# Performance work log

Hardware: AMD Instinct MI355X
Metric: run time of the kernel (lower is better)

The kernel has to match this reference:

```python
import jax, jax.numpy as jnp
import numpy as np

STEP = 5
ALPHA = 0.01
D = 1024
BN_EPS = 1e-5
L2_EPS = 1e-12


def setup_inputs() -> dict:
    key = jax.random.key(0)
    k1, k2 = jax.random.split(key, 2)
    B = 16
    x = jax.random.normal(k1, (B * STEP, D), dtype=jnp.float32)
    W = jax.random.normal(k2, (D, D), dtype=jnp.float32) * 0.02
    b = jnp.zeros((D,), jnp.float32)
    gamma = jnp.ones((D,), jnp.float32)
    beta = jnp.zeros((D,), jnp.float32)
    return {"x": x, "W": W, "b": b, "gamma": gamma, "beta": beta}


def reference(x, W, b, gamma, beta):
    BS = x.shape[0]          # B * STEP
    B = BS // STEP
    x_seq = x.reshape(B, STEP, D)

    def step_fn(h, xt):
        # xt: [B, D]; Hebbian fast-weight update
        # hebb = alpha * (k v^T - k^2 * h)
        hebb = ALPHA * (xt[:, :, None] * xt[:, None, :] - (xt ** 2)[:, :, None] * h)
        h = h + hebb
        return h, h

    h0 = jnp.zeros((B, D, D), x.dtype)
    _, mems = jax.lax.scan(step_fn, h0, jnp.swapaxes(x_seq, 0, 1))  # [STEP, B, D, D]
    # torch.cat(memory_total, dim=0) -> step-major stacking
    mem = mems.reshape(BS, D, D)

    # batched mat-vec readout; x here is batch-major (faithful to original mismatch)
    q = jnp.einsum('nij,nj->ni', mem, x)  # [BS, D]

    y = q @ W.T + b
    # BatchNorm1d in training mode: batch statistics, biased variance
    mu = y.mean(axis=0)
    var = y.var(axis=0)
    yhat = (y - mu) / jnp.sqrt(var + BN_EPS)
    out = jax.nn.relu(yhat * gamma + beta)
    # F.normalize: L2 over dim=1 with eps clamp
    norm = jnp.linalg.norm(out, axis=1, keepdims=True)
    return out / jnp.maximum(norm, L2_EPS)
```

## Files before the change

### kernel.cpp

```cpp
#include <hip/hip_runtime.h>
#include <hip/hip_bf16.h>
#include <math.h>

#define D_DIM   1024
#define BS      80
#define BATCH   16
#define STEPS   5
#define ALPHA   0.01f
#define BN_EPS  1e-5f
#define L2_EPS  1e-12f

#define K2_NN   8
#define K2_NG   (BS / K2_NN)

__global__ __launch_bounds__(256) void k1_q(const float* __restrict__ x,
                                            float* __restrict__ q,
                                            float* __restrict__ colsum,
                                            float* __restrict__ colsumsq) {
    const int n    = blockIdx.x;
    const int tid  = threadIdx.x;
    const int lane = tid & 63;
    const int wid  = tid >> 6;
    const int t    = n >> 4;
    const int bb   = n & 15;

    if (n < 8) {
        colsum  [n * 256 + tid] = 0.f;
    } else if (n < 16) {
        colsumsq[(n - 8) * 256 + tid] = 0.f;
    }

    const float4* __restrict__ xv = (const float4*)(x + (size_t)n * D_DIM);
    const float4 v = xv[tid];

    float4 k[STEPS];
#pragma unroll
    for (int s = 0; s < STEPS; ++s)
        k[s] = ((const float4*)(x + (size_t)(bb * STEPS + s) * D_DIM))[tid];

    float p[STEPS];
#pragma unroll
    for (int s = 0; s < STEPS; ++s)
        p[s] = k[s].x * v.x + k[s].y * v.y + k[s].z * v.z + k[s].w * v.w;

#pragma unroll
    for (int off = 32; off; off >>= 1) {
#pragma unroll
        for (int s = 0; s < STEPS; ++s) p[s] += __shfl_xor(p[s], off, 64);
    }

    __shared__ float sh[4][STEPS];
    if (lane == 0) {
#pragma unroll
        for (int s = 0; s < STEPS; ++s) sh[wid][s] = p[s];
    }
    __syncthreads();
    float c[STEPS];
#pragma unroll
    for (int s = 0; s < STEPS; ++s)
        c[s] = sh[0][s] + sh[1][s] + sh[2][s] + sh[3][s];

    float4 acc = make_float4(0.f, 0.f, 0.f, 0.f);
    for (int s = 0; s <= t; ++s) {
        const float4 xs = k[s];
        acc.x = acc.x * (1.f - ALPHA * xs.x * xs.x) + c[s] * xs.x;
        acc.y = acc.y * (1.f - ALPHA * xs.y * xs.y) + c[s] * xs.y;
        acc.z = acc.z * (1.f - ALPHA * xs.z * xs.z) + c[s] * xs.z;
        acc.w = acc.w * (1.f - ALPHA * xs.w * xs.w) + c[s] * xs.w;
    }
    acc.x *= ALPHA; acc.y *= ALPHA; acc.z *= ALPHA; acc.w *= ALPHA;
    ((float4*)(q + (size_t)n * D_DIM))[tid] = acc;
}

__global__ __launch_bounds__(256) void k2_gemm(const float* __restrict__ q,
                                               const float* __restrict__ W,
                                               const float* __restrict__ bvec,
                                               float* __restrict__ y,
                                               float* __restrict__ colsum,
                                               float* __restrict__ colsumsq) {
    const int tid  = threadIdx.x;
    const int lane = tid & 63;
    const int wid  = tid >> 6;
    const int wave = blockIdx.x * 4 + wid;
    const int jg   = wave & 255;
    const int ng   = wave >> 8;
    const int j0   = jg * 4;
    const int n0   = ng * K2_NN;

    const float4* __restrict__ W4 = (const float4*)W;
    const float4* __restrict__ q4 = (const float4*)q;

    float4 w[4][4];
#pragma unroll
    for (int jj = 0; jj < 4; ++jj)
#pragma unroll
        for (int m = 0; m < 4; ++m)
            w[jj][m] = W4[(size_t)(j0 + jj) * 256 + lane + 64 * m];

    const float4 b4 = ((const float4*)bvec)[jg];

    float csum[4] = {0.f, 0.f, 0.f, 0.f};
    float csq [4] = {0.f, 0.f, 0.f, 0.f};

#pragma unroll 2
    for (int nn = 0; nn < K2_NN; ++nn) {
        const int n = n0 + nn;
        float4 qv[4];
#pragma unroll
        for (int m = 0; m < 4; ++m)
            qv[m] = q4[(size_t)n * 256 + lane + 64 * m];

        float s[4] = {0.f, 0.f, 0.f, 0.f};
#pragma unroll
        for (int jj = 0; jj < 4; ++jj) {
#pragma unroll
            for (int m = 0; m < 4; ++m) {
                s[jj] += w[jj][m].x * qv[m].x + w[jj][m].y * qv[m].y
                       + w[jj][m].z * qv[m].z + w[jj][m].w * qv[m].w;
            }
        }
#pragma unroll
        for (int off = 32; off; off >>= 1) {
#pragma unroll
            for (int jj = 0; jj < 4; ++jj) s[jj] += __shfl_xor(s[jj], off, 64);
        }
        if (lane == 0) {
            float4 yv = make_float4(s[0] + b4.x, s[1] + b4.y,
                                    s[2] + b4.z, s[3] + b4.w);
            ((float4*)y)[(size_t)n * 256 + jg] = yv;
            csum[0] += yv.x; csum[1] += yv.y; csum[2] += yv.z; csum[3] += yv.w;
            csq[0] += yv.x * yv.x; csq[1] += yv.y * yv.y;
            csq[2] += yv.z * yv.z; csq[3] += yv.w * yv.w;
        }
    }
    if (lane == 0) {
#pragma unroll
        for (int jj = 0; jj < 4; ++jj) {
            atomicAdd(&colsum [j0 + jj], csum[jj]);
            atomicAdd(&colsumsq[j0 + jj], csq[jj]);
        }
    }
}

__global__ __launch_bounds__(256) void k4_norm(const float* __restrict__ y,
                                               const float* __restrict__ colsum,
                                               const float* __restrict__ colsumsq,
                                               const float* __restrict__ gamma,
                                               const float* __restrict__ beta,
                                               float* __restrict__ out) {
    const int n   = blockIdx.x;
    const int tid = threadIdx.x;

    const float inv_bs = 1.f / (float)BS;

    float o[4];
    float ss = 0.f;
#pragma unroll
    for (int m = 0; m < 4; ++m) {
        const int j = tid + 256 * m;
        const float mu   = colsum[j] * inv_bs;
        const float var  = colsumsq[j] * inv_bs - mu * mu;
        const float istd = rsqrtf(var + BN_EPS);
        float v = (y[(size_t)n * D_DIM + j] - mu) * istd * gamma[j] + beta[j];
        v = fmaxf(v, 0.f);
        o[m] = v;
        ss += v * v;
    }

#pragma unroll
    for (int off = 32; off; off >>= 1) ss += __shfl_xor(ss, off, 64);
    __shared__ float sred[4];
    if ((tid & 63) == 0) sred[tid >> 6] = ss;
    __syncthreads();
    const float stot = sred[0] + sred[1] + sred[2] + sred[3];

    const float scale = 1.f / fmaxf(sqrtf(stot), L2_EPS);
#pragma unroll
    for (int m = 0; m < 4; ++m)
        out[(size_t)n * D_DIM + tid + 256 * m] = o[m] * scale;
}

extern "C" void kernel_launch(void* const* d_in, const int* in_sizes, int n_in,
                              void* d_out, int out_size, void* d_ws, size_t ws_size,
                              hipStream_t stream) {
    const float* x     = (const float*)d_in[0];
    const float* W     = (const float*)d_in[1];
    const float* bvec  = (const float*)d_in[2];
    const float* gamma = (const float*)d_in[3];
    const float* beta  = (const float*)d_in[4];

    float* q        = (float*)d_ws;
    float* y        = q + BS * D_DIM;
    float* colsum   = y + BS * D_DIM;
    float* colsumsq = colsum + D_DIM;

    float* out = (float*)d_out;

    k1_q   <<<BS,                    256, 0, stream>>>(x, q, colsum, colsumsq);
    k2_gemm<<<(256 * K2_NG) / 4,     256, 0, stream>>>(q, W, bvec, y, colsum, colsumsq);
    k4_norm<<<BS,                    256, 0, stream>>>(y, colsum, colsumsq, gamma, beta, out);
}
```

Baseline: 80.46 us.

## Fuse three kernels into one cooperative kernel with grid-wide syncs

Merges the q-readout, GEMM with BN stats, and normalization kernels into a single cooperative launch of 256 blocks of 512 threads, separated by grid.sync(). Each GEMM wave now handles 10 rows instead of 8, and the first and last phases use float2 per thread. The aim is to remove two kernel launch gaps. In exchange it pays for grid barriers, and it depends on colsum and colsumsq being zeroed by the four blocks that write 2048 contiguous floats covering both arrays.

```diff
diff --git a/kernel.cpp b/kernel.cpp
--- a/kernel.cpp
+++ b/kernel.cpp
@@ -1,183 +1,184 @@
 #include <hip/hip_runtime.h>
-#include <hip/hip_bf16.h>
+#include <hip/hip_cooperative_groups.h>
 #include <math.h>
+
+namespace cg = cooperative_groups;
 
 #define D_DIM   1024
 #define BS      80
-#define BATCH   16
 #define STEPS   5
 #define ALPHA   0.01f
 #define BN_EPS  1e-5f
 #define L2_EPS  1e-12f
 
-#define K2_NN   8
-#define K2_NG   (BS / K2_NN)
-
-__global__ __launch_bounds__(256) void k1_q(const float* __restrict__ x,
-                                            float* __restrict__ q,
-                                            float* __restrict__ colsum,
-                                            float* __restrict__ colsumsq) {
-    const int n    = blockIdx.x;
+#define NBLK    256
+#define NTHR    512
+
+__global__ __launch_bounds__(NTHR) void fused_all(
+        const float* __restrict__ x,
+        const float* __restrict__ W,
+        const float* __restrict__ bvec,
+        const float* __restrict__ gamma,
+        const float* __restrict__ beta,
+        float* __restrict__ out,
+        float* __restrict__ q,
+        float* __restrict__ y,
+        float* __restrict__ colsum,
+        float* __restrict__ colsumsq) {
+    cg::grid_group grid = cg::this_grid();
+
     const int tid  = threadIdx.x;
     const int lane = tid & 63;
     const int wid  = tid >> 6;
-    const int t    = n >> 4;
-    const int bb   = n & 15;
-
-    if (n < 8) {
-        colsum  [n * 256 + tid] = 0.f;
-    } else if (n < 16) {
-        colsumsq[(n - 8) * 256 + tid] = 0.f;
+    const int blk  = blockIdx.x;
+
+    __shared__ float sh1[8][STEPS];
+    __shared__ float sr[8];
+
+    if (blk < 4) colsum[blk * NTHR + tid] = 0.f;
+
+    if (blk < BS) {
+        const int n  = blk;
+        const int t  = n >> 4;
+        const int bb = n & 15;
+
+        const float2 v = ((const float2*)(x + (size_t)n * D_DIM))[tid];
+
+        float2 k[STEPS];
+#pragma unroll
+        for (int s = 0; s < STEPS; ++s)
+            k[s] = ((const float2*)(x + (size_t)(bb * STEPS + s) * D_DIM))[tid];
+
+        float p[STEPS];
+#pragma unroll
+        for (int s = 0; s < STEPS; ++s)
+            p[s] = k[s].x * v.x + k[s].y * v.y;
+
+#pragma unroll
+        for (int off = 32; off; off >>= 1) {
+#pragma unroll
+            for (int s = 0; s < STEPS; ++s) p[s] += __shfl_xor(p[s], off, 64);
+        }
+        if (lane == 0) {
+#pragma unroll
+            for (int s = 0; s < STEPS; ++s) sh1[wid][s] = p[s];
+        }
+        __syncthreads();
+        float c[STEPS];
+#pragma unroll
+        for (int s = 0; s < STEPS; ++s) {
+            float acc = 0.f;
+#pragma unroll
+            for (int w = 0; w < 8; ++w) acc += sh1[w][s];
+            c[s] = acc;
+        }
+
+        float2 acc = make_float2(0.f, 0.f);
+        for (int s = 0; s <= t; ++s) {
+            const float2 xs = k[s];
+            acc.x = acc.x * (1.f - ALPHA * xs.x * xs.x) + c[s] * xs.x;
+            acc.y = acc.y * (1.f - ALPHA * xs.y * xs.y) + c[s] * xs.y;
+        }
+        acc.x *= ALPHA; acc.y *= ALPHA;
+        ((float2*)(q + (size_t)n * D_DIM))[tid] = acc;
     }
 
-    const float4* __restrict__ xv = (const float4*)(x + (size_t)n * D_DIM);
-    const float4 v = xv[tid];
-
-    float4 k[STEPS];
-#pragma unroll
-    for (int s = 0; s < STEPS; ++s)
-        k[s] = ((const float4*)(x + (size_t)(bb * STEPS + s) * D_DIM))[tid];
-
-    float p[STEPS];
-#pragma unroll
-    for (int s = 0; s < STEPS; ++s)
-        p[s] = k[s].x * v.x + k[s].y * v.y + k[s].z * v.z + k[s].w * v.w;
-
-#pragma unroll
-    for (int off = 32; off; off >>= 1) {
-#pragma unroll
-        for (int s = 0; s < STEPS; ++s) p[s] += __shfl_xor(p[s], off, 64);
+    grid.sync();
+
+    {
+        const int gwave = blk * 8 + wid;
+        const int jg    = gwave & 255;
+        const int ng    = gwave >> 8;
+        const int j0    = jg * 4;
+        const int n0    = ng * 10;
+
+        const float4* __restrict__ W4 = (const float4*)W;
+        const float4* __restrict__ q4 = (const float4*)q;
+
+        float4 w[4][4];
+#pragma unroll
+        for (int jj = 0; jj < 4; ++jj)
+#pragma unroll
+            for (int m = 0; m < 4; ++m)
+                w[jj][m] = W4[(size_t)(j0 + jj) * 256 + lane + 64 * m];
+
+        const float4 b4 = ((const float4*)bvec)[jg];
+
+        float csum[4] = {0.f, 0.f, 0.f, 0.f};
+        float csq [4] = {0.f, 0.f, 0.f, 0.f};
+
+        for (int nn = 0; nn < 10; ++nn) {
+            const int n = n0 + nn;
+            float4 qv[4];
+#pragma unroll
+            for (int m = 0; m < 4; ++m)
+                qv[m] = q4[(size_t)n * 256 + lane + 64 * m];
+
+            float s[4] = {0.f, 0.f, 0.f, 0.f};
+#pragma unroll
+            for (int jj = 0; jj < 4; ++jj) {
+#pragma unroll
+                for (int m = 0; m < 4; ++m) {
+                    s[jj] += w[jj][m].x * qv[m].x + w[jj][m].y * qv[m].y
+                           + w[jj][m].z * qv[m].z + w[jj][m].w * qv[m].w;
+                }
+            }
+#pragma unroll
+            for (int off = 32; off; off >>= 1) {
+#pragma unroll
+                for (int jj = 0; jj < 4; ++jj) s[jj] += __shfl_xor(s[jj], off, 64);
+            }
+            if (lane == 0) {
+                float4 yv = make_float4(s[0] + b4.x, s[1] + b4.y,
+                                        s[2] + b4.z, s[3] + b4.w);
+                ((float4*)y)[(size_t)n * 256 + jg] = yv;
+                csum[0] += yv.x; csum[1] += yv.y; csum[2] += yv.z; csum[3] += yv.w;
+                csq[0] += yv.x * yv.x; csq[1] += yv.y * yv.y;
+                csq[2] += yv.z * yv.z; csq[3] += yv.w * yv.w;
+            }
+        }
+        if (lane == 0) {
+#pragma unroll
+            for (int jj = 0; jj < 4; ++jj) {
+                atomicAdd(&colsum  [j0 + jj], csum[jj]);
+                atomicAdd(&colsumsq[j0 + jj], csq[jj]);
+            }
+        }
     }
 
-    __shared__ float sh[4][STEPS];
-    if (lane == 0) {
-#pragma unroll
-        for (int s = 0; s < STEPS; ++s) sh[wid][s] = p[s];
+    grid.sync();
+
+    if (blk < BS) {
+        const int n = blk;
+        const float inv_bs = 1.f / (float)BS;
+
+        float o[2];
+        float ss = 0.f;
+#pragma unroll
+        for (int m = 0; m < 2; ++m) {
+            const int j = tid + NTHR * m;
+            const float mu   = colsum[j] * inv_bs;
+            const float var  = colsumsq[j] * inv_bs - mu * mu;
+            const float istd = rsqrtf(var + BN_EPS);
+            float v = (y[(size_t)n * D_DIM + j] - mu) * istd * gamma[j] + beta[j];
+            v = fmaxf(v, 0.f);
+            o[m] = v;
+            ss += v * v;
+        }
+
+#pragma unroll
+        for (int off = 32; off; off >>= 1) ss += __shfl_xor(ss, off, 64);
+        if (lane == 0) sr[wid] = ss;
+        __syncthreads();
+        float stot = 0.f;
+#pragma unroll
+        for (int w = 0; w < 8; ++w) stot += sr[w];
+
+        const float scale = 1.f / fmaxf(sqrtf(stot), L2_EPS);
+#pragma unroll
+        for (int m = 0; m < 2; ++m)
+            out[(size_t)n * D_DIM + tid + NTHR * m] = o[m] * scale;
     }
-    __syncthreads();
-    float c[STEPS];
-#pragma unroll
-    for (int s = 0; s < STEPS; ++s)
-        c[s] = sh[0][s] + sh[1][s] + sh[2][s] + sh[3][s];
-
-    float4 acc = make_float4(0.f, 0.f, 0.f, 0.f);
-    for (int s = 0; s <= t; ++s) {
-        const float4 xs = k[s];
-        acc.x = acc.x * (1.f - ALPHA * xs.x * xs.x) + c[s] * xs.x;
-        acc.y = acc.y * (1.f - ALPHA * xs.y * xs.y) + c[s] * xs.y;
-        acc.z = acc.z * (1.f - ALPHA * xs.z * xs.z) + c[s] * xs.z;
-        acc.w = acc.w * (1.f - ALPHA * xs.w * xs.w) + c[s] * xs.w;
-    }
-    acc.x *= ALPHA; acc.y *= ALPHA; acc.z *= ALPHA; acc.w *= ALPHA;
-    ((float4*)(q + (size_t)n * D_DIM))[tid] = acc;
-}
-
-__global__ __launch_bounds__(256) void k2_gemm(const float* __restrict__ q,
-                                               const float* __restrict__ W,
-                                               const float* __restrict__ bvec,
-                                               float* __restrict__ y,
-                                               float* __restrict__ colsum,
-                                               float* __restrict__ colsumsq) {
-    const int tid  = threadIdx.x;
-    const int lane = tid & 63;
-    const int wid  = tid >> 6;
-    const int wave = blockIdx.x * 4 + wid;
-    const int jg   = wave & 255;
-    const int ng   = wave >> 8;
-    const int j0   = jg * 4;
-    const int n0   = ng * K2_NN;
-
-    const float4* __restrict__ W4 = (const float4*)W;
-    const float4* __restrict__ q4 = (const float4*)q;
-
-    float4 w[4][4];
-#pragma unroll
-    for (int jj = 0; jj < 4; ++jj)
-#pragma unroll
-        for (int m = 0; m < 4; ++m)
-            w[jj][m] = W4[(size_t)(j0 + jj) * 256 + lane + 64 * m];
-
-    const float4 b4 = ((const float4*)bvec)[jg];
-
-    float csum[4] = {0.f, 0.f, 0.f, 0.f};
-    float csq [4] = {0.f, 0.f, 0.f, 0.f};
-
-#pragma unroll 2
-    for (int nn = 0; nn < K2_NN; ++nn) {
-        const int n = n0 + nn;
-        float4 qv[4];
-#pragma unroll
-        for (int m = 0; m < 4; ++m)
-            qv[m] = q4[(size_t)n * 256 + lane + 64 * m];
-
-        float s[4] = {0.f, 0.f, 0.f, 0.f};
-#pragma unroll
-        for (int jj = 0; jj < 4; ++jj) {
-#pragma unroll
-            for (int m = 0; m < 4; ++m) {
-                s[jj] += w[jj][m].x * qv[m].x + w[jj][m].y * qv[m].y
-                       + w[jj][m].z * qv[m].z + w[jj][m].w * qv[m].w;
-            }
-        }
-#pragma unroll
-        for (int off = 32; off; off >>= 1) {
-#pragma unroll
-            for (int jj = 0; jj < 4; ++jj) s[jj] += __shfl_xor(s[jj], off, 64);
-        }
-        if (lane == 0) {
-            float4 yv = make_float4(s[0] + b4.x, s[1] + b4.y,
-                                    s[2] + b4.z, s[3] + b4.w);
-            ((float4*)y)[(size_t)n * 256 + jg] = yv;
-            csum[0] += yv.x; csum[1] += yv.y; csum[2] += yv.z; csum[3] += yv.w;
-            csq[0] += yv.x * yv.x; csq[1] += yv.y * yv.y;
-            csq[2] += yv.z * yv.z; csq[3] += yv.w * yv.w;
-        }
-    }
-    if (lane == 0) {
-#pragma unroll
-        for (int jj = 0; jj < 4; ++jj) {
-            atomicAdd(&colsum [j0 + jj], csum[jj]);
-            atomicAdd(&colsumsq[j0 + jj], csq[jj]);
-        }
-    }
-}
-
-__global__ __launch_bounds__(256) void k4_norm(const float* __restrict__ y,
-                                               const float* __restrict__ colsum,
-                                               const float* __restrict__ colsumsq,
-                                               const float* __restrict__ gamma,
-                                               const float* __restrict__ beta,
-                                               float* __restrict__ out) {
-    const int n   = blockIdx.x;
-    const int tid = threadIdx.x;
-
-    const float inv_bs = 1.f / (float)BS;
-
-    float o[4];
-    float ss = 0.f;
-#pragma unroll
-    for (int m = 0; m < 4; ++m) {
-        const int j = tid + 256 * m;
-        const float mu   = colsum[j] * inv_bs;
-        const float var  = colsumsq[j] * inv_bs - mu * mu;
-        const float istd = rsqrtf(var + BN_EPS);
-        float v = (y[(size_t)n * D_DIM + j] - mu) * istd * gamma[j] + beta[j];
-        v = fmaxf(v, 0.f);
-        o[m] = v;
-        ss += v * v;
-    }
-
-#pragma unroll
-    for (int off = 32; off; off >>= 1) ss += __shfl_xor(ss, off, 64);
-    __shared__ float sred[4];
-    if ((tid & 63) == 0) sred[tid >> 6] = ss;
-    __syncthreads();
-    const float stot = sred[0] + sred[1] + sred[2] + sred[3];
-
-    const float scale = 1.f / fmaxf(sqrtf(stot), L2_EPS);
-#pragma unroll
-    for (int m = 0; m < 4; ++m)
-        out[(size_t)n * D_DIM + tid + 256 * m] = o[m] * scale;
 }
 
 extern "C" void kernel_launch(void* const* d_in, const int* in_sizes, int n_in,
@@ -196,7 +197,9 @@
 
     float* out = (float*)d_out;
 
-    k1_q   <<<BS,                    256, 0, stream>>>(x, q, colsum, colsumsq);
-    k2_gemm<<<(256 * K2_NG) / 4,     256, 0, stream>>>(q, W, bvec, y, colsum, colsumsq);
-    k4_norm<<<BS,                    256, 0, stream>>>(y, colsum, colsumsq, gamma, beta, out);
+    void* args[] = {(void*)&x, (void*)&W, (void*)&bvec, (void*)&gamma,
+                    (void*)&beta, (void*)&out, (void*)&q, (void*)&y,
+                    (void*)&colsum, (void*)&colsumsq};
+    hipLaunchCooperativeKernel((const void*)fused_all, dim3(NBLK), dim3(NTHR),
+                               args, 0, stream);
 }
```

Result: slower. 145.3 us (+80.6%).

## Fuse q computation into GEMM kernel and compute BN stats in norm kernel

Applied to the files above, without the earlier changes.

Merges the q readout kernel into the GEMM kernel: each block recomputes q for 10 rows into shared memory and then multiplies them against a 32-column slice of W. The atomic column-statistics accumulation is removed, and the norm kernel instead has each block reread all 80 rows of y to compute the column mean and variance. This removes one launch, the q round trip through global memory and the atomics. In exchange, q is recomputed 32 times per row across blocks and y is read redundantly 80 times in the norm kernel.

```diff
diff --git a/kernel.cpp b/kernel.cpp
--- a/kernel.cpp
+++ b/kernel.cpp
@@ -1,95 +1,83 @@
 #include <hip/hip_runtime.h>
-#include <hip/hip_bf16.h>
 #include <math.h>
 
 #define D_DIM   1024
 #define BS      80
-#define BATCH   16
 #define STEPS   5
 #define ALPHA   0.01f
 #define BN_EPS  1e-5f
 #define L2_EPS  1e-12f
 
-#define K2_NN   8
-#define K2_NG   (BS / K2_NN)
+__global__ __launch_bounds__(512) void kA(const float* __restrict__ x,
+                                          const float* __restrict__ W,
+                                          const float* __restrict__ bvec,
+                                          float* __restrict__ y) {
+    __shared__ float4 qs[10 * 256];
 
-__global__ __launch_bounds__(256) void k1_q(const float* __restrict__ x,
-                                            float* __restrict__ q,
-                                            float* __restrict__ colsum,
-                                            float* __restrict__ colsumsq) {
-    const int n    = blockIdx.x;
-    const int tid  = threadIdx.x;
-    const int lane = tid & 63;
-    const int wid  = tid >> 6;
-    const int t    = n >> 4;
-    const int bb   = n & 15;
+    const int tid    = threadIdx.x;
+    const int lane   = tid & 63;
+    const int wid    = tid >> 6;
+    const int blk    = blockIdx.x;
+    const int jslice = blk & 31;
+    const int ng     = blk >> 5;
+    const int n0     = ng * 10;
 
-    if (n < 8) {
-        colsum  [n * 256 + tid] = 0.f;
-    } else if (n < 16) {
-        colsumsq[(n - 8) * 256 + tid] = 0.f;
-    }
+    for (int r = wid; r < 10; r += 8) {
+        const int n  = n0 + r;
+        const int t  = n >> 4;
+        const int bb = n & 15;
 
-    const float4* __restrict__ xv = (const float4*)(x + (size_t)n * D_DIM);
-    const float4 v = xv[tid];
+        const float4* __restrict__ xv = (const float4*)(x + (size_t)n * D_DIM);
+        float4 v[4];
+#pragma unroll
+        for (int m = 0; m < 4; ++m) v[m] = xv[lane + 64 * m];
 
-    float4 k[STEPS];
+        float4 k[STEPS][4];
 #pragma unroll
-    for (int s = 0; s < STEPS; ++s)
-        k[s] = ((const float4*)(x + (size_t)(bb * STEPS + s) * D_DIM))[tid];
+        for (int s = 0; s < STEPS; ++s) {
+            const float4* __restrict__ xk =
+                (const float4*)(x + (size_t)(bb * STEPS + s) * D_DIM);
+#pragma unroll
+            for (int m = 0; m < 4; ++m) k[s][m] = xk[lane + 64 * m];
+        }
 
-    float p[STEPS];
+        float p[STEPS];
 #pragma unroll
-    for (int s = 0; s < STEPS; ++s)
-        p[s] = k[s].x * v.x + k[s].y * v.y + k[s].z * v.z + k[s].w * v.w;
+        for (int s = 0; s < STEPS; ++s) {
+            float acc = 0.f;
+#pragma unroll
+            for (int m = 0; m < 4; ++m) {
+                acc += k[s][m].x * v[m].x + k[s][m].y * v[m].y
+                     + k[s][m].z * v[m].z + k[s][m].w * v[m].w;
+            }
+            p[s] = acc;
+        }
+#pragma unroll
+        for (int off = 32; off; off >>= 1) {
+#pragma unroll
+            for (int s = 0; s < STEPS; ++s) p[s] += __shfl_xor(p[s], off, 64);
+        }
 
 #pragma unroll
-    for (int off = 32; off; off >>= 1) {
-#pragma unroll
-        for (int s = 0; s < STEPS; ++s) p[s] += __shfl_xor(p[s], off, 64);
-    }
-
-    __shared__ float sh[4][STEPS];
-    if (lane == 0) {
-#pragma unroll
-        for (int s = 0; s < STEPS; ++s) sh[wid][s] = p[s];
+        for (int m = 0; m < 4; ++m) {
+            float4 acc = make_float4(0.f, 0.f, 0.f, 0.f);
+            for (int s = 0; s <= t; ++s) {
+                const float4 xs = k[s][m];
+                const float  cs = p[s];
+                acc.x = acc.x * (1.f - ALPHA * xs.x * xs.x) + cs * xs.x;
+                acc.y = acc.y * (1.f - ALPHA * xs.y * xs.y) + cs * xs.y;
+                acc.z = acc.z * (1.f - ALPHA * xs.z * xs.z) + cs * xs.z;
+                acc.w = acc.w * (1.f - ALPHA * xs.w * xs.w) + cs * xs.w;
+            }
+            acc.x *= ALPHA; acc.y *= ALPHA; acc.z *= ALPHA; acc.w *= ALPHA;
+            qs[r * 256 + lane + 64 * m] = acc;
+        }
     }
     __syncthreads();
-    float c[STEPS];
-#pragma unroll
-    for (int s = 0; s < STEPS; ++s)
-        c[s] = sh[0][s] + sh[1][s] + sh[2][s] + sh[3][s];
 
-    float4 acc = make_float4(0.f, 0.f, 0.f, 0.f);
-    for (int s = 0; s <= t; ++s) {
-        const float4 xs = k[s];
-        acc.x = acc.x * (1.f - ALPHA * xs.x * xs.x) + c[s] * xs.x;
-        acc.y = acc.y * (1.f - ALPHA * xs.y * xs.y) + c[s] * xs.y;
-        acc.z = acc.z * (1.f - ALPHA * xs.z * xs.z) + c[s] * xs.z;
-        acc.w = acc.w * (1.f - ALPHA * xs.w * xs.w) + c[s] * xs.w;
-    }
-    acc.x *= ALPHA; acc.y *= ALPHA; acc.z *= ALPHA; acc.w *= ALPHA;
-    ((float4*)(q + (size_t)n * D_DIM))[tid] = acc;
-}
-
-__global__ __launch_bounds__(256) void k2_gemm(const float* __restrict__ q,
-                                               const float* __restrict__ W,
-                                               const float* __restrict__ bvec,
-                                               float* __restrict__ y,
-                                               float* __restrict__ colsum,
-                                               float* __restrict__ colsumsq) {
-    const int tid  = threadIdx.x;
-    const int lane = tid & 63;
-    const int wid  = tid >> 6;
-    const int wave = blockIdx.x * 4 + wid;
-    const int jg   = wave & 255;
-    const int ng   = wave >> 8;
-    const int j0   = jg * 4;
-    const int n0   = ng * K2_NN;
+    const int j0 = jslice * 32 + wid * 4;
 
     const float4* __restrict__ W4 = (const float4*)W;
-    const float4* __restrict__ q4 = (const float4*)q;
-
     float4 w[4][4];
 #pragma unroll
     for (int jj = 0; jj < 4; ++jj)
@@ -97,18 +85,12 @@
         for (int m = 0; m < 4; ++m)
             w[jj][m] = W4[(size_t)(j0 + jj) * 256 + lane + 64 * m];
 
-    const float4 b4 = ((const float4*)bvec)[jg];
+    const float4 b4 = ((const float4*)bvec)[j0 >> 2];
 
-    float csum[4] = {0.f, 0.f, 0.f, 0.f};
-    float csq [4] = {0.f, 0.f, 0.f, 0.f};
-
-#pragma unroll 2
-    for (int nn = 0; nn < K2_NN; ++nn) {
-        const int n = n0 + nn;
+    for (int nn = 0; nn < 10; ++nn) {
         float4 qv[4];
 #pragma unroll
-        for (int m = 0; m < 4; ++m)
-            qv[m] = q4[(size_t)n * 256 + lane + 64 * m];
+        for (int m = 0; m < 4; ++m) qv[m] = qs[nn * 256 + lane + 64 * m];
 
         float s[4] = {0.f, 0.f, 0.f, 0.f};
 #pragma unroll
@@ -125,48 +107,52 @@
             for (int jj = 0; jj < 4; ++jj) s[jj] += __shfl_xor(s[jj], off, 64);
         }
         if (lane == 0) {
-            float4 yv = make_float4(s[0] + b4.x, s[1] + b4.y,
-                                    s[2] + b4.z, s[3] + b4.w);
-            ((float4*)y)[(size_t)n * 256 + jg] = yv;
-            csum[0] += yv.x; csum[1] += yv.y; csum[2] += yv.z; csum[3] += yv.w;
-            csq[0] += yv.x * yv.x; csq[1] += yv.y * yv.y;
-            csq[2] += yv.z * yv.z; csq[3] += yv.w * yv.w;
-        }
-    }
-    if (lane == 0) {
-#pragma unroll
-        for (int jj = 0; jj < 4; ++jj) {
-            atomicAdd(&colsum [j0 + jj], csum[jj]);
-            atomicAdd(&colsumsq[j0 + jj], csq[jj]);
+            ((float4*)y)[(size_t)(n0 + nn) * 256 + (j0 >> 2)] =
+                make_float4(s[0] + b4.x, s[1] + b4.y, s[2] + b4.z, s[3] + b4.w);
         }
     }
 }
 
-__global__ __launch_bounds__(256) void k4_norm(const float* __restrict__ y,
-                                               const float* __restrict__ colsum,
-                                               const float* __restrict__ colsumsq,
-                                               const float* __restrict__ gamma,
-                                               const float* __restrict__ beta,
-                                               float* __restrict__ out) {
+__global__ __launch_bounds__(256) void kB(const float* __restrict__ y,
+                                          const float* __restrict__ gamma,
+                                          const float* __restrict__ beta,
+                                          float* __restrict__ out) {
     const int n   = blockIdx.x;
     const int tid = threadIdx.x;
 
-    const float inv_bs = 1.f / (float)BS;
+    const float4* __restrict__ y4 = (const float4*)y;
 
-    float o[4];
-    float ss = 0.f;
-#pragma unroll
-    for (int m = 0; m < 4; ++m) {
-        const int j = tid + 256 * m;
-        const float mu   = colsum[j] * inv_bs;
-        const float var  = colsumsq[j] * inv_bs - mu * mu;
-        const float istd = rsqrtf(var + BN_EPS);
-        float v = (y[(size_t)n * D_DIM + j] - mu) * istd * gamma[j] + beta[j];
-        v = fmaxf(v, 0.f);
-        o[m] = v;
-        ss += v * v;
+    float4 sum  = make_float4(0.f, 0.f, 0.f, 0.f);
+    float4 sq   = make_float4(0.f, 0.f, 0.f, 0.f);
+    float4 mine = make_float4(0.f, 0.f, 0.f, 0.f);
+#pragma unroll 8
+    for (int r = 0; r < BS; ++r) {
+        const float4 v = y4[(size_t)r * 256 + tid];
+        if (r == n) mine = v;
+        sum.x += v.x; sum.y += v.y; sum.z += v.z; sum.w += v.w;
+        sq.x += v.x * v.x; sq.y += v.y * v.y;
+        sq.z += v.z * v.z; sq.w += v.w * v.w;
     }
 
+    const float inv_bs = 1.f / (float)BS;
+    const float4 g4 = ((const float4*)gamma)[tid];
+    const float4 be4 = ((const float4*)beta)[tid];
+
+    float4 o;
+    {
+        const float mux = sum.x * inv_bs, muy = sum.y * inv_bs;
+        const float muz = sum.z * inv_bs, muw = sum.w * inv_bs;
+        const float ix = rsqrtf(sq.x * inv_bs - mux * mux + BN_EPS);
+        const float iy = rsqrtf(sq.y * inv_bs - muy * muy + BN_EPS);
+        const float iz = rsqrtf(sq.z * inv_bs - muz * muz + BN_EPS);
+        const float iw = rsqrtf(sq.w * inv_bs - muw * muw + BN_EPS);
+        o.x = fmaxf((mine.x - mux) * ix * g4.x + be4.x, 0.f);
+        o.y = fmaxf((mine.y - muy) * iy * g4.y + be4.y, 0.f);
+        o.z = fmaxf((mine.z - muz) * iz * g4.z + be4.z, 0.f);
+        o.w = fmaxf((mine.w - muw) * iw * g4.w + be4.w, 0.f);
+    }
+
+    float ss = o.x * o.x + o.y * o.y + o.z * o.z + o.w * o.w;
 #pragma unroll
     for (int off = 32; off; off >>= 1) ss += __shfl_xor(ss, off, 64);
     __shared__ float sred[4];
@@ -175,9 +161,8 @@
     const float stot = sred[0] + sred[1] + sred[2] + sred[3];
 
     const float scale = 1.f / fmaxf(sqrtf(stot), L2_EPS);
-#pragma unroll
-    for (int m = 0; m < 4; ++m)
-        out[(size_t)n * D_DIM + tid + 256 * m] = o[m] * scale;
+    o.x *= scale; o.y *= scale; o.z *= scale; o.w *= scale;
+    ((float4*)out)[(size_t)n * 256 + tid] = o;
 }
 
 extern "C" void kernel_launch(void* const* d_in, const int* in_sizes, int n_in,
@@ -189,14 +174,9 @@
     const float* gamma = (const float*)d_in[3];
     const float* beta  = (const float*)d_in[4];
 
-    float* q        = (float*)d_ws;
-    float* y        = q + BS * D_DIM;
-    float* colsum   = y + BS * D_DIM;
-    float* colsumsq = colsum + D_DIM;
-
+    float* y   = (float*)d_ws;
     float* out = (float*)d_out;
 
-    k1_q   <<<BS,                    256, 0, stream>>>(x, q, colsum, colsumsq);
-    k2_gemm<<<(256 * K2_NG) / 4,     256, 0, stream>>>(q, W, bvec, y, colsum, colsumsq);
-    k4_norm<<<BS,                    256, 0, stream>>>(y, colsum, colsumsq, gamma, beta, out);
+    kA<<<256, 512, 0, stream>>>(x, W, bvec, y);
+    kB<<<BS,  256, 0, stream>>>(y, gamma, beta, out);
 }
```

After: 115.2 us. +43.2%, slower.
